# Optimization experiments

Hardware: AMD Instinct MI355X
Metric: run time of the kernel (lower is better)

The kernel has to match this reference:

```python
import jax, jax.numpy as jnp
import numpy as np

B, N, DIM = 2, 2048, 1024
H, KVH, DH = 16, 4, 64
SCALE = DH ** -0.5


def setup_inputs() -> dict:
    key = jax.random.key(0)
    ks = jax.random.split(key, 7)
    x = jax.random.normal(ks[0], (B, N, DIM), dtype=jnp.float32)
    mask = jax.random.randint(ks[1], (N, N), 0, 2).astype(jnp.bool_)
    Wq = jax.random.normal(ks[2], (DIM, H * DH), dtype=jnp.float32) * (DIM ** -0.5)
    Wk = jax.random.normal(ks[3], (DIM, KVH * DH), dtype=jnp.float32) * (DIM ** -0.5)
    Wv = jax.random.normal(ks[4], (DIM, KVH * DH), dtype=jnp.float32) * (DIM ** -0.5)
    Wo = jax.random.normal(ks[5], (H * DH, DIM), dtype=jnp.float32) * ((H * DH) ** -0.5)
    bo = jnp.zeros((DIM,), dtype=jnp.float32)
    return {"x": x, "mask": mask, "Wq": Wq, "Wk": Wk, "Wv": Wv, "Wo": Wo, "bo": bo}


def reference(x, mask, Wq, Wk, Wv, Wo, bo):
    b, n, _ = x.shape
    # projections -> [b, h, n, dh]
    q = (x @ Wq).reshape(b, n, H, DH).transpose(0, 2, 1, 3)
    k = (x @ Wk).reshape(b, n, KVH, DH).transpose(0, 2, 1, 3)
    v = (x @ Wv).reshape(b, n, KVH, DH).transpose(0, 2, 1, 3)
    # GQA: repeat kv heads, 'b h n d -> b (h r) n d'
    r = H // KVH
    k = jnp.repeat(k, r, axis=1)
    v = jnp.repeat(v, r, axis=1)
    dots = jnp.einsum('bhnd,bhmd->bhnm', q, k) * SCALE  # [b,h,n,n]
    dots = jnp.where(mask, jnp.float32(-1e9), dots)
    attn = jax.nn.softmax(dots, axis=-1)  # dropout p=0.0 -> identity
    out = jnp.einsum('bhnm,bhmd->bhnd', attn, v)
    out = out.transpose(0, 2, 1, 3).reshape(b, n, H * DH)
    return out @ Wo + bo
```

## Files before the change

### kernel.cpp

```cpp
#include <hip/hip_runtime.h>
#include <stdint.h>

typedef unsigned short u16;
typedef u16 u16x8 __attribute__((ext_vector_type(8)));
typedef u16 u16x4 __attribute__((ext_vector_type(4)));
typedef float f32x4 __attribute__((ext_vector_type(4)));

#define AS1(p) ((const __attribute__((address_space(1))) void*)(p))
#define AS3(p) ((__attribute__((address_space(3))) void*)(p))

__device__ __forceinline__ void gload16(void* lds, const void* g) {
  __builtin_amdgcn_global_load_lds(AS1(g), AS3(lds), 16, 0, 0);
}

__device__ __forceinline__ u16 f2bf(float f) {
  union { float f; uint32_t u; } c; c.f = f;
  uint32_t u = c.u + 0x7FFFu + ((c.u >> 16) & 1u);
  return (u16)(u >> 16);
}

__device__ __forceinline__ void mfma16(f32x4& d, u16x8 a, u16x8 b) {
  asm("v_mfma_f32_16x16x32_bf16 %0, %1, %2, %0" : "+v"(d) : "v"(a), "v"(b));
}

__global__ void prep(const float* __restrict__ x, u16* __restrict__ xb,
                     const void* __restrict__ mraw, unsigned long long* __restrict__ mb,
                     const float* __restrict__ Wq, const float* __restrict__ Wk,
                     const float* __restrict__ Wv, const float* __restrict__ Wo,
                     u16* __restrict__ Wcat, u16* __restrict__ WoT) {
  __shared__ float t[64][65];
  const int bi = blockIdx.x, tid = threadIdx.x;
  if (bi < 4096) {
    int i = (bi * 256 + tid) * 4;
    float4 v = *(const float4*)(x + i);
    u16x4 o; o.x = f2bf(v.x); o.y = f2bf(v.y); o.z = f2bf(v.z); o.w = f2bf(v.w);
    *(u16x4*)(xb + i) = o;
  } else if (bi < 20480) {
    const int lane = tid & 63;
    const uint32_t* mi = (const uint32_t*)mraw;
    const bool int_mode = __all(mi[lane] <= 1u);
    const int wid = ((bi - 4096) * 256 + tid) >> 6;
    const size_t base = (size_t)(wid >> 5) * 2048 + (size_t)(wid & 31) * 64 + lane;
    bool bit;
    if (int_mode) bit = mi[base] != 0;
    else          bit = ((const uint8_t*)mraw)[base] != 0;
    unsigned long long bm = __ballot(bit);
    if (lane == 0) mb[wid] = bm;
  } else {
    const float* in; u16* out; int R, C, bx, by, lb;
    if (bi < 20736)      { lb = bi - 20480; in = Wq; out = Wcat;              R = 1024; C = 1024; bx = lb & 15; by = lb >> 4; }
    else if (bi < 20800) { lb = bi - 20736; in = Wk; out = Wcat + 1024*1024;  R = 1024; C = 256;  bx = lb & 3;  by = lb >> 2; }
    else if (bi < 20864) { lb = bi - 20800; in = Wv; out = Wcat + 1280*1024;  R = 1024; C = 256;  bx = lb & 3;  by = lb >> 2; }
    else                 { lb = bi - 20864; in = Wo; out = WoT;               R = 1024; C = 1024; bx = lb & 15; by = lb >> 4; }
    const int c0 = bx * 64, r0 = by * 64;
#pragma unroll
    for (int k = 0; k < 4; ++k) {
      int idx = k * 256 + tid;
      int r = idx >> 4, c = (idx & 15) * 4;
      float4 v = *(const float4*)(in + (size_t)(r0 + r) * C + c0 + c);
      t[r][c] = v.x; t[r][c + 1] = v.y; t[r][c + 2] = v.z; t[r][c + 3] = v.w;
    }
    __syncthreads();
#pragma unroll
    for (int k = 0; k < 4; ++k) {
      int idx = k * 256 + tid;
      int c = idx >> 4, r = (idx & 15) * 4;
      u16x4 o;
      o.x = f2bf(t[r][c]); o.y = f2bf(t[r + 1][c]);
      o.z = f2bf(t[r + 2][c]); o.w = f2bf(t[r + 3][c]);
      *(u16x4*)(out + (size_t)(c0 + c) * R + r0 + r) = o;
    }
  }
}

#define SCALE_LOG2 0.18033688011112042f

template <int EPI, int BM, int BN>
__global__ __launch_bounds__(256, 2) void gemm_bt(
    const u16* __restrict__ A, const u16* __restrict__ Bt,
    u16* __restrict__ Qb, u16* __restrict__ Kb, u16* __restrict__ VTb,
    float* __restrict__ Co, const float* __restrict__ bias) {
  constexpr int MR = BM / 32, NR = BN / 32;
  __shared__ u16 As[BM * 32];
  __shared__ u16 Bs[BN * 32];
  const int tid = threadIdx.x, lane = tid & 63, wave = tid >> 6;
  const int wr = wave >> 1, wc = wave & 1;
  const int lg = lane >> 4, ll = lane & 15;
  const int bm = blockIdx.x * BM, bn = blockIdx.y * BN;
  const int K = 1024;
  const u16* Ag = A + (size_t)bm * K;
  const u16* Bg = Bt + (size_t)bn * K;

  f32x4 acc[MR][NR];
#pragma unroll
  for (int m = 0; m < MR; ++m)
#pragma unroll
    for (int n = 0; n < NR; ++n) acc[m][n] = f32x4{0.f, 0.f, 0.f, 0.f};

  const int r0 = tid >> 2, c0 = (tid & 3) * 8;

  for (int k0 = 0; k0 < K; k0 += 32) {
    gload16(&As[(size_t)tid * 8], Ag + (size_t)r0 * K + k0 + c0);
    if constexpr (BM == 128)
      gload16(&As[(size_t)(256 + tid) * 8], Ag + (size_t)(64 + r0) * K + k0 + c0);
    gload16(&Bs[(size_t)tid * 8], Bg + (size_t)r0 * K + k0 + c0);
    if constexpr (BN == 128)
      gload16(&Bs[(size_t)(256 + tid) * 8], Bg + (size_t)(64 + r0) * K + k0 + c0);
    __syncthreads();
    u16x8 af[MR], bf[NR];
#pragma unroll
    for (int m = 0; m < MR; ++m) af[m] = *(const u16x8*)&As[(wr * (BM/2) + m * 16 + ll) * 32 + lg * 8];
#pragma unroll
    for (int n = 0; n < NR; ++n) bf[n] = *(const u16x8*)&Bs[(wc * (BN/2) + n * 16 + ll) * 32 + lg * 8];
#pragma unroll
    for (int m = 0; m < MR; ++m)
#pragma unroll
      for (int n = 0; n < NR; ++n) mfma16(acc[m][n], af[m], bf[n]);
    __syncthreads();
  }

  const int row0 = bm + wr * (BM/2) + lg * 4;
  const int col0 = bn + wc * (BN/2) + ll;
#pragma unroll
  for (int m = 0; m < MR; ++m) {
#pragma unroll
    for (int n = 0; n < NR; ++n) {
      const int col = col0 + n * 16;
#pragma unroll
      for (int r = 0; r < 4; ++r) {
        const int row = row0 + m * 16 + r;
        const float v = acc[m][n][r];
        if (EPI == 0) {
          const int b = row >> 11, t = row & 2047;
          if (col < 1024) {
            Qb[((size_t)(b * 16 + (col >> 6)) * 2048 + t) * 64 + (col & 63)] = f2bf(v * SCALE_LOG2);
          } else if (col < 1280) {
            const int c2 = col - 1024;
            Kb[((size_t)(b * 4 + (c2 >> 6)) * 2048 + t) * 64 + (c2 & 63)] = f2bf(v);
          } else {
            const int c2 = col - 1280;
            VTb[((size_t)(b * 4 + (c2 >> 6)) * 64 + (c2 & 63)) * 2048 + t] = f2bf(v);
          }
        } else {
          Co[(size_t)row * 1024 + col] = v + bias[col];
        }
      }
    }
  }
}


__device__ __forceinline__ void stage_kv(u16* Kl, u16* Vl,
                                         const u16* Kg, const u16* Vg,
                                         int kv0, int tid) {
  const int i0 = tid, i1 = 256 + tid;
  const int ra = i0 >> 3, sa = (i0 & 7) ^ (ra & 7);
  const int rb = i1 >> 3, sb = (i1 & 7) ^ (rb & 7);
  gload16(&Kl[(size_t)i0 * 8], Kg + (size_t)(kv0 + ra) * 64 + sa * 8);
  gload16(&Kl[(size_t)i1 * 8], Kg + (size_t)(kv0 + rb) * 64 + sb * 8);
  gload16(&Vl[(size_t)i0 * 8], Vg + (size_t)ra * 2048 + kv0 + sa * 8);
  gload16(&Vl[(size_t)i1 * 8], Vg + (size_t)rb * 2048 + kv0 + sb * 8);
}

__global__ __launch_bounds__(256, 2) void attn(
    const u16* __restrict__ Qb, const u16* __restrict__ Kb, const u16* __restrict__ VTb,
    const unsigned long long* __restrict__ mb, u16* __restrict__ Ob) {
  __shared__ u16 Klds[2][64 * 64];
  __shared__ u16 Vlds[2][64 * 64];
  __shared__ u16 Plds[4][32 * 64];
  const int tid = threadIdx.x, lane = tid & 63, wave = tid >> 6;
  const int lg = lane >> 4, ll = lane & 15;
  const int qt = blockIdx.x, h = blockIdx.y, b = blockIdx.z;
  const int kvh = h >> 2;
  const u16* Qg = Qb + ((size_t)(b * 16 + h) * 2048 + qt * 128 + wave * 32) * 64;
  const u16* Kg = Kb + (size_t)(b * 4 + kvh) * 2048 * 64;
  const u16* Vg = VTb + (size_t)(b * 4 + kvh) * 64 * 2048;
  u16* Pw = Plds[wave];
  const int sw = (ll & 7) << 3;

  u16x8 qf[2][2];
#pragma unroll
  for (int qb2 = 0; qb2 < 2; ++qb2)
#pragma unroll
    for (int kc = 0; kc < 2; ++kc)
      qf[qb2][kc] = *(const u16x8*)&Qg[(qb2 * 16 + ll) * 64 + kc * 32 + lg * 8];

  f32x4 o[2][4];
#pragma unroll
  for (int qb2 = 0; qb2 < 2; ++qb2)
#pragma unroll
    for (int db = 0; db < 4; ++db) o[qb2][db] = f32x4{0.f, 0.f, 0.f, 0.f};
  float mx[2] = {-3e9f, -3e9f}, ls[2] = {0.f, 0.f};
  const int qrow0 = qt * 128 + wave * 32;

  stage_kv(Klds[0], Vlds[0], Kg, Vg, 0, tid);

  for (int c = 0; c < 32; ++c) {
    const int cur = c & 1;
    const u16* Kl = Klds[cur];
    const u16* Vl = Vlds[cur];
    const unsigned long long w0 = mb[(size_t)(qrow0 + ll) * 32 + c];
    const unsigned long long w1 = mb[(size_t)(qrow0 + 16 + ll) * 32 + c];
    if (c < 31) {
      stage_kv(Klds[cur ^ 1], Vlds[cur ^ 1], Kg, Vg, (c + 1) * 64, tid);
      asm volatile("s_waitcnt vmcnt(4)" ::: "memory");
    } else {
      asm volatile("s_waitcnt vmcnt(0)" ::: "memory");
    }
    __builtin_amdgcn_s_barrier();
    asm volatile("" ::: "memory");

    f32x4 sf[2][4];
#pragma unroll
    for (int qb2 = 0; qb2 < 2; ++qb2)
#pragma unroll
      for (int kt = 0; kt < 4; ++kt) sf[qb2][kt] = f32x4{0.f, 0.f, 0.f, 0.f};
#pragma unroll
    for (int kt = 0; kt < 4; ++kt) {
      const int krow = kt * 16 + ll;
#pragma unroll
      for (int kc = 0; kc < 2; ++kc) {
        u16x8 kf = *(const u16x8*)&Kl[(krow * 64 + kc * 32 + lg * 8) ^ ((krow & 7) << 3)];
        mfma16(sf[0][kt], kf, qf[0][kc]);
        mfma16(sf[1][kt], kf, qf[1][kc]);
      }
    }

    float p[2][4][4], smax[2];
#pragma unroll
    for (int qb2 = 0; qb2 < 2; ++qb2) {
      const unsigned long long w = qb2 ? w1 : w0;
      float m0 = -3e9f;
#pragma unroll
      for (int kt = 0; kt < 4; ++kt)
#pragma unroll
        for (int r = 0; r < 4; ++r) {
          float s = sf[qb2][kt][r];
          s = ((w >> (kt * 16 + lg * 4 + r)) & 1ull) ? -3e9f : s;
          p[qb2][kt][r] = s;
          m0 = fmaxf(m0, s);
        }
      m0 = fmaxf(m0, __shfl_xor(m0, 16));
      m0 = fmaxf(m0, __shfl_xor(m0, 32));
      smax[qb2] = m0;
    }

    const bool upd = (smax[0] > mx[0] + 8.f) || (smax[1] > mx[1] + 8.f);
    if (__any(upd)) {
      float av[2];
#pragma unroll
      for (int qb2 = 0; qb2 < 2; ++qb2) {
        const float mn = fmaxf(mx[qb2], smax[qb2]);
        av[qb2] = exp2f(mx[qb2] - mn);
        mx[qb2] = mn;
        ls[qb2] *= av[qb2];
      }
#pragma unroll
      for (int r = 0; r < 4; ++r) {
        const float a0 = __shfl(av[0], lg * 4 + r);
        const float a1 = __shfl(av[1], lg * 4 + r);
#pragma unroll
        for (int db = 0; db < 4; ++db) { o[0][db][r] *= a0; o[1][db][r] *= a1; }
      }
    }

#pragma unroll
    for (int qb2 = 0; qb2 < 2; ++qb2) {
      const int q = qb2 * 16 + ll;
      float psum = 0.f;
#pragma unroll
      for (int kt = 0; kt < 4; ++kt) {
        float e0 = exp2f(p[qb2][kt][0] - mx[qb2]);
        float e1 = exp2f(p[qb2][kt][1] - mx[qb2]);
        float e2 = exp2f(p[qb2][kt][2] - mx[qb2]);
        float e3 = exp2f(p[qb2][kt][3] - mx[qb2]);
        psum += (e0 + e1) + (e2 + e3);
        u16x4 pk; pk.x = f2bf(e0); pk.y = f2bf(e1); pk.z = f2bf(e2); pk.w = f2bf(e3);
        *(u16x4*)&Pw[q * 64 + ((kt * 16 + lg * 4) ^ sw)] = pk;
      }
      psum += __shfl_xor(psum, 16);
      psum += __shfl_xor(psum, 32);
      ls[qb2] += psum;
    }

    asm volatile("" ::: "memory");
    __builtin_amdgcn_sched_barrier(0);

#pragma unroll
    for (int kc = 0; kc < 2; ++kc) {
      u16x8 pf[2];
#pragma unroll
      for (int qb2 = 0; qb2 < 2; ++qb2) {
        const int q = qb2 * 16 + ll;
        pf[qb2] = *(const u16x8*)&Pw[q * 64 + ((kc * 32 + lg * 8) ^ sw)];
      }
#pragma unroll
      for (int db = 0; db < 4; ++db) {
        const int d = db * 16 + ll;
        u16x8 vf = *(const u16x8*)&Vl[(d * 64 + kc * 32 + lg * 8) ^ ((d & 7) << 3)];
        mfma16(o[0][db], pf[0], vf);
        mfma16(o[1][db], pf[1], vf);
      }
    }
    asm volatile("s_waitcnt lgkmcnt(0)" ::: "memory");
    __builtin_amdgcn_s_barrier();
    asm volatile("" ::: "memory");
  }

#pragma unroll
  for (int qb2 = 0; qb2 < 2; ++qb2) {
#pragma unroll
    for (int r = 0; r < 4; ++r) {
      const float lsr = __shfl(ls[qb2], lg * 4 + r);
      const float inv = 1.f / lsr;
      const int tok = qt * 128 + wave * 32 + qb2 * 16 + lg * 4 + r;
#pragma unroll
      for (int db = 0; db < 4; ++db)
        Ob[(size_t)(b * 2048 + tok) * 1024 + h * 64 + db * 16 + ll] = f2bf(o[qb2][db][r] * inv);
    }
  }
}

extern "C" void kernel_launch(void* const* d_in, const int* in_sizes, int n_in,
                              void* d_out, int out_size, void* d_ws, size_t ws_size,
                              hipStream_t stream) {
  const float* x  = (const float*)d_in[0];
  const void*  mk = d_in[1];
  const float* Wq = (const float*)d_in[2];
  const float* Wk = (const float*)d_in[3];
  const float* Wv = (const float*)d_in[4];
  const float* Wo = (const float*)d_in[5];
  const float* bo = (const float*)d_in[6];
  float* out = (float*)d_out;

  char* ws = (char*)d_ws;
  size_t off = 0;
  auto alloc = [&](size_t bytes) { void* p = ws + off; off += (bytes + 255) & ~(size_t)255; return p; };
  u16* xb   = (u16*)alloc(4096ull * 1024 * 2);
  u16* Wcat = (u16*)alloc(1536ull * 1024 * 2);
  u16* WoT  = (u16*)alloc(1024ull * 1024 * 2);
  u16* Qb   = (u16*)alloc(2ull * 16 * 2048 * 64 * 2);
  u16* Kb   = (u16*)alloc(2ull * 4 * 2048 * 64 * 2);
  u16* VTb  = (u16*)alloc(2ull * 4 * 64 * 2048 * 2);
  u16* Ob   = (u16*)alloc(4096ull * 1024 * 2);
  unsigned long long* mbits = (unsigned long long*)alloc(65536ull * 8);
  (void)ws_size; (void)in_sizes; (void)n_in; (void)out_size;

  prep<<<21120, 256, 0, stream>>>(x, xb, mk, mbits, Wq, Wk, Wv, Wo, Wcat, WoT);
  gemm_bt<0, 64, 128><<<dim3(64, 12), 256, 0, stream>>>(xb, Wcat, Qb, Kb, VTb, nullptr, nullptr);
  attn<<<dim3(16, 16, 2), 256, 0, stream>>>(Qb, Kb, VTb, mbits, Ob);
  gemm_bt<1, 128, 64><<<dim3(32, 16), 256, 0, stream>>>(Ob, WoT, nullptr, nullptr, nullptr, out, bo);
}
```

Before: 157.5 us.

## Split attention KV range in two and merge partials with combine kernel

Splits each attention block's 32 KV chunks into two halves run by separate blocks, doubling the grid from 512 to 1024 blocks. Each half writes unnormalized bf16 partial outputs plus the running max and sum, and a new combine kernel merges them with log-sum-exp rescaling. This aims to raise occupancy and CU utilization on a GPU with many CUs. The cost is an extra kernel launch, extra global traffic for the partials, and extra bf16 rounding of the intermediate outputs. It falls back to the old path when the workspace is too small.

```diff
diff --git a/kernel.cpp b/kernel.cpp
--- a/kernel.cpp
+++ b/kernel.cpp
@@ -17,6 +17,10 @@
   union { float f; uint32_t u; } c; c.f = f;
   uint32_t u = c.u + 0x7FFFu + ((c.u >> 16) & 1u);
   return (u16)(u >> 16);
+}
+
+__device__ __forceinline__ float bf2f(u16 h) {
+  union { uint32_t u; float f; } c; c.u = ((uint32_t)h) << 16; return c.f;
 }
 
 __device__ __forceinline__ void mfma16(f32x4& d, u16x8 a, u16x8 b) {
@@ -162,15 +166,21 @@
   gload16(&Vl[(size_t)i1 * 8], Vg + (size_t)rb * 2048 + kv0 + sb * 8);
 }
 
+template <int SPLIT>
 __global__ __launch_bounds__(256, 2) void attn(
     const u16* __restrict__ Qb, const u16* __restrict__ Kb, const u16* __restrict__ VTb,
-    const unsigned long long* __restrict__ mb, u16* __restrict__ Ob) {
+    const unsigned long long* __restrict__ mb, u16* __restrict__ Ob,
+    u16* __restrict__ PO, float* __restrict__ PM, float* __restrict__ PL) {
   __shared__ u16 Klds[2][64 * 64];
   __shared__ u16 Vlds[2][64 * 64];
   __shared__ u16 Plds[4][32 * 64];
   const int tid = threadIdx.x, lane = tid & 63, wave = tid >> 6;
   const int lg = lane >> 4, ll = lane & 15;
-  const int qt = blockIdx.x, h = blockIdx.y, b = blockIdx.z;
+  const int qt = blockIdx.x, h = blockIdx.y;
+  const int b = SPLIT ? (blockIdx.z >> 1) : blockIdx.z;
+  const int s = SPLIT ? (blockIdx.z & 1) : 0;
+  const int cbeg = SPLIT ? s * 16 : 0;
+  const int cend = SPLIT ? cbeg + 16 : 32;
   const int kvh = h >> 2;
   const u16* Qg = Qb + ((size_t)(b * 16 + h) * 2048 + qt * 128 + wave * 32) * 64;
   const u16* Kg = Kb + (size_t)(b * 4 + kvh) * 2048 * 64;
@@ -193,15 +203,15 @@
   float mx[2] = {-3e9f, -3e9f}, ls[2] = {0.f, 0.f};
   const int qrow0 = qt * 128 + wave * 32;
 
-  stage_kv(Klds[0], Vlds[0], Kg, Vg, 0, tid);
-
-  for (int c = 0; c < 32; ++c) {
+  stage_kv(Klds[0], Vlds[0], Kg, Vg, cbeg * 64, tid);
+
+  for (int c = cbeg; c < cend; ++c) {
     const int cur = c & 1;
     const u16* Kl = Klds[cur];
     const u16* Vl = Vlds[cur];
     const unsigned long long w0 = mb[(size_t)(qrow0 + ll) * 32 + c];
     const unsigned long long w1 = mb[(size_t)(qrow0 + 16 + ll) * 32 + c];
-    if (c < 31) {
+    if (c < cend - 1) {
       stage_kv(Klds[cur ^ 1], Vlds[cur ^ 1], Kg, Vg, (c + 1) * 64, tid);
       asm volatile("s_waitcnt vmcnt(4)" ::: "memory");
     } else {
@@ -235,10 +245,10 @@
       for (int kt = 0; kt < 4; ++kt)
 #pragma unroll
         for (int r = 0; r < 4; ++r) {
-          float s = sf[qb2][kt][r];
-          s = ((w >> (kt * 16 + lg * 4 + r)) & 1ull) ? -3e9f : s;
-          p[qb2][kt][r] = s;
-          m0 = fmaxf(m0, s);
+          float sv = sf[qb2][kt][r];
+          sv = ((w >> (kt * 16 + lg * 4 + r)) & 1ull) ? -3e9f : sv;
+          p[qb2][kt][r] = sv;
+          m0 = fmaxf(m0, sv);
         }
       m0 = fmaxf(m0, __shfl_xor(m0, 16));
       m0 = fmaxf(m0, __shfl_xor(m0, 32));
@@ -307,18 +317,59 @@
     asm volatile("" ::: "memory");
   }
 
-#pragma unroll
-  for (int qb2 = 0; qb2 < 2; ++qb2) {
-#pragma unroll
-    for (int r = 0; r < 4; ++r) {
-      const float lsr = __shfl(ls[qb2], lg * 4 + r);
-      const float inv = 1.f / lsr;
-      const int tok = qt * 128 + wave * 32 + qb2 * 16 + lg * 4 + r;
-#pragma unroll
-      for (int db = 0; db < 4; ++db)
-        Ob[(size_t)(b * 2048 + tok) * 1024 + h * 64 + db * 16 + ll] = f2bf(o[qb2][db][r] * inv);
-    }
-  }
+  if (SPLIT == 0) {
+#pragma unroll
+    for (int qb2 = 0; qb2 < 2; ++qb2) {
+#pragma unroll
+      for (int r = 0; r < 4; ++r) {
+        const float lsr = __shfl(ls[qb2], lg * 4 + r);
+        const float inv = 1.f / lsr;
+        const int tok = qt * 128 + wave * 32 + qb2 * 16 + lg * 4 + r;
+#pragma unroll
+        for (int db = 0; db < 4; ++db)
+          Ob[(size_t)(b * 2048 + tok) * 1024 + h * 64 + db * 16 + ll] = f2bf(o[qb2][db][r] * inv);
+      }
+    }
+  } else {
+    const size_t rowbase = (((size_t)s * 2 + b) * 16 + h) * 2048;
+#pragma unroll
+    for (int qb2 = 0; qb2 < 2; ++qb2) {
+#pragma unroll
+      for (int r = 0; r < 4; ++r) {
+        const int tok = qt * 128 + wave * 32 + qb2 * 16 + lg * 4 + r;
+#pragma unroll
+        for (int db = 0; db < 4; ++db)
+          PO[(rowbase + tok) * 64 + db * 16 + ll] = f2bf(o[qb2][db][r]);
+      }
+      if (lane < 16) {
+        const int tok = qt * 128 + wave * 32 + qb2 * 16 + lane;
+        PM[rowbase + tok] = mx[qb2];
+        PL[rowbase + tok] = ls[qb2];
+      }
+    }
+  }
+}
+
+__global__ void combine(const u16* __restrict__ PO, const float* __restrict__ PM,
+                        const float* __restrict__ PL, u16* __restrict__ Ob) {
+  const size_t i = (size_t)blockIdx.x * 256 + threadIdx.x;
+  const size_t row = i >> 3;
+  const int d0 = (int)(i & 7) * 8;
+  const size_t SSTR = 65536ull;
+  const float m1 = PM[row], m2 = PM[row + SSTR];
+  const float l1 = PL[row], l2 = PL[row + SSTR];
+  const float m = fmaxf(m1, m2);
+  const float a1 = exp2f(m1 - m), a2 = exp2f(m2 - m);
+  const float inv = 1.f / (a1 * l1 + a2 * l2);
+  u16x8 x1 = *(const u16x8*)&PO[row * 64 + d0];
+  u16x8 x2 = *(const u16x8*)&PO[SSTR * 64 + row * 64 + d0];
+  const size_t bh = row >> 11, tok = row & 2047;
+  const size_t b = bh >> 4, h = bh & 15;
+  u16x8 rr;
+#pragma unroll
+  for (int j = 0; j < 8; ++j)
+    rr[j] = f2bf((a1 * bf2f(x1[j]) + a2 * bf2f(x2[j])) * inv);
+  *(u16x8*)&Ob[(b * 2048 + tok) * 1024 + h * 64 + d0] = rr;
 }
 
 extern "C" void kernel_launch(void* const* d_in, const int* in_sizes, int n_in,
@@ -344,10 +395,19 @@
   u16* VTb  = (u16*)alloc(2ull * 4 * 64 * 2048 * 2);
   u16* Ob   = (u16*)alloc(4096ull * 1024 * 2);
   unsigned long long* mbits = (unsigned long long*)alloc(65536ull * 8);
-  (void)ws_size; (void)in_sizes; (void)n_in; (void)out_size;
+  u16*   PO = (u16*)alloc(2ull * 65536 * 64 * 2);
+  float* PM = (float*)alloc(2ull * 65536 * 4);
+  float* PL = (float*)alloc(2ull * 65536 * 4);
+  const bool use_split = (off <= ws_size);
+  (void)in_sizes; (void)n_in; (void)out_size;
 
   prep<<<21120, 256, 0, stream>>>(x, xb, mk, mbits, Wq, Wk, Wv, Wo, Wcat, WoT);
   gemm_bt<0, 64, 128><<<dim3(64, 12), 256, 0, stream>>>(xb, Wcat, Qb, Kb, VTb, nullptr, nullptr);
-  attn<<<dim3(16, 16, 2), 256, 0, stream>>>(Qb, Kb, VTb, mbits, Ob);
+  if (use_split) {
+    attn<1><<<dim3(16, 16, 4), 256, 0, stream>>>(Qb, Kb, VTb, mbits, nullptr, PO, PM, PL);
+    combine<<<2048, 256, 0, stream>>>(PO, PM, PL, Ob);
+  } else {
+    attn<0><<<dim3(16, 16, 2), 256, 0, stream>>>(Qb, Kb, VTb, mbits, Ob, nullptr, nullptr, nullptr);
+  }
   gemm_bt<1, 128, 64><<<dim3(32, 16), 256, 0, stream>>>(Ob, WoT, nullptr, nullptr, nullptr, out, bo);
 }
```

After: 160.6 us. Within noise of the previous version (+2.0%).
